# Kernel optimization log

Measured on AMD Instinct MI355X. Metric: run time of the kernel, lower is better.

## Reference

```python
import jax, jax.numpy as jnp
import numpy as np

NX = 2048
NL = 20
BATCH = 512
EIGMAX = 10.0
EPS = 1e-9


def prox_cardan(eta, x):
    """Prox of u -> -eta*(log(u)+log(1-u)) at x: unique root in (0,1) of
    u^3 - (1+x)u^2 + (x-2eta)u + eta = 0 (Cardano / trigonometric method)."""
    b = -(1.0 + x)
    c = x - 2.0 * eta
    d = eta
    p = c - b * b / 3.0
    q = 2.0 * b ** 3 / 27.0 - b * c / 3.0 + d
    disc = -4.0 * p ** 3 - 27.0 * q ** 2
    # three-real-roots branch (trigonometric); requires p<0
    pm = jnp.minimum(p, -1e-12)
    m = 2.0 * jnp.sqrt(-pm / 3.0)
    arg = jnp.clip(3.0 * q / (pm * m), -1.0, 1.0)
    th = jnp.arccos(arg)
    k = jnp.arange(3, dtype=x.dtype)
    t_trig = m[..., None] * jnp.cos((th[..., None] - 2.0 * jnp.pi * k) / 3.0)
    r_trig = t_trig - b[..., None] / 3.0
    in01 = (r_trig > 0.0) & (r_trig < 1.0)
    idx = jnp.argmax(in01, axis=-1)
    root3 = jnp.take_along_axis(r_trig, idx[..., None], axis=-1)[..., 0]
    # one-real-root branch
    s = jnp.sqrt(jnp.maximum(q * q / 4.0 + p ** 3 / 27.0, 0.0))
    root1 = jnp.cbrt(-q / 2.0 + s) + jnp.cbrt(-q / 2.0 - s) - b / 3.0
    u = jnp.where(disc >= 0.0, root3, root1)
    return jnp.clip(u, EPS, 1.0 - EPS)


def setup_inputs() -> dict:
    key = jax.random.key(0)
    k1, k2, k3, k4, k5 = jax.random.split(key, 5)
    x = jax.random.uniform(k1, (BATCH, 1, NX), dtype=jnp.float32)
    # symmetric PSD operators for T^T T and D^T D (as in a discretized inverse problem)
    A = jax.random.normal(k2, (NX, NX), dtype=jnp.float32)
    tTT = (A @ A.T) / NX
    B = jax.random.normal(k3, (NX, NX), dtype=jnp.float32)
    tDD = (B @ B.T) / NX
    # orthogonal change-of-basis: element <-> eigen bases
    Q, _ = jnp.linalg.qr(jax.random.normal(k4, (NX, NX), dtype=jnp.float32))
    Pelt = Q.astype(jnp.float32)
    Peig = Q.T.astype(jnp.float32)
    x_b = jnp.einsum('ij,bcj->bci', tTT, x) + 0.01 * jax.random.normal(k5, (BATCH, 1, NX), dtype=jnp.float32)
    gamma = jnp.full((NL,), 0.1, dtype=jnp.float32)   # nn.Parameter([0.1])
    mu = jnp.zeros((NL,), dtype=jnp.float32)          # nn.Parameter([0.0])
    reg = jnp.full((NL,), 0.001, dtype=jnp.float32)   # noisy=True -> trainable 0.001
    return {"x": x, "x_b": x_b, "tDD": tDD, "tTT": tTT, "Peig": Peig,
            "Pelt": Pelt, "gamma": gamma, "mu": mu, "reg": reg}


def reference(x, x_b, tDD, tTT, Peig, Pelt, gamma, mu, reg):
    def step(xc, params):
        g_raw, mu_raw, reg_raw = params
        g = jax.nn.softplus(g_raw)
        mu_l = jax.nn.softplus(mu_raw) / 1e6
        reg_l = jax.nn.softplus(reg_raw) / (EIGMAX ** 2)
        grad = (jnp.einsum('ij,bcj->bci', tTT, xc) - x_b
                + reg_l * jnp.einsum('ij,bcj->bci', tDD, xc))
        xt = xc - g * grad
        xt = jnp.einsum('ij,bcj->bci', Pelt, xt)
        xt = prox_cardan(g * mu_l, xt)
        xt = jnp.einsum('ij,bcj->bci', Peig, xt)
        return xt, None

    out, _ = jax.lax.scan(step, x, (gamma, mu, reg))
    return out
```

## Files before the change

kernel.cpp:

```cpp
#include <hip/hip_runtime.h>
#include <math.h>

#define MDIM 512
#define NDIM 2048
#define KDIM 2048
#define NLAYERS 20

static const size_t MN = (size_t)MDIM * NDIM;
static const size_t OPN = (size_t)KDIM * KDIM;

using bf16x8 = __attribute__((ext_vector_type(8))) short;
using f32x4  = __attribute__((ext_vector_type(4))) float;

__device__ __forceinline__ double softplusd(double v) {
    return (v > 20.0) ? v : log1p(exp(v));
}

__device__ __forceinline__ float prox_cardan_f(float eta, float x) {
    const float b  = -(1.0f + x);
    const float c  = x - 2.0f * eta;
    const float dd = eta;
    const float p  = c - b * b * (1.0f / 3.0f);
    const float q  = 2.0f * b * b * b * (1.0f / 27.0f) - b * c * (1.0f / 3.0f) + dd;
    const float disc = -4.0f * p * p * p - 27.0f * q * q;
    const float pm = fminf(p, -1e-12f);
    const float mm = 2.0f * sqrtf(-pm * (1.0f / 3.0f));
    float arg = 3.0f * q / (pm * mm);
    arg = fminf(fmaxf(arg, -1.0f), 1.0f);
    const float th = acosf(arg);
    const float TWO_PI = 6.28318530717958647692f;
    const float r0 = mm * cosf(th * (1.0f / 3.0f)) - b * (1.0f / 3.0f);
    const float r1 = mm * cosf((th - TWO_PI) * (1.0f / 3.0f)) - b * (1.0f / 3.0f);
    const float r2 = mm * cosf((th - 2.0f * TWO_PI) * (1.0f / 3.0f)) - b * (1.0f / 3.0f);
    const bool in0 = (r0 > 0.0f) && (r0 < 1.0f);
    const bool in1 = (r1 > 0.0f) && (r1 < 1.0f);
    const bool in2 = (r2 > 0.0f) && (r2 < 1.0f);
    const float root3 = in0 ? r0 : (in1 ? r1 : (in2 ? r2 : r0));
    const float s = sqrtf(fmaxf(q * q * 0.25f + p * p * p * (1.0f / 27.0f), 0.0f));
    const float root1 = cbrtf(-q * 0.5f + s) + cbrtf(-q * 0.5f - s) - b * (1.0f / 3.0f);
    const float u = (disc >= 0.0f) ? root3 : root1;
    return fminf(fmaxf(u, 1e-9f), 1.0f - 1e-9f);
}

__device__ __forceinline__ double prox_newton_d(double eta, double x) {
    double u = (double)prox_cardan_f((float)eta, (float)x);
#pragma unroll
    for (int i = 0; i < 4; ++i) {
        const double um1 = u - 1.0;
        const double umx = u - x;
        const double P  = u * um1 * umx - eta * (2.0 * u - 1.0);
        const double dP = um1 * umx + u * umx + u * um1 - 2.0 * eta;
        u = u - P / dP;
        u = fmin(fmax(u, 1e-12), 1.0 - 1e-12);
    }
    return fmin(fmax(u, 1e-9), 1.0 - 1e-9);
}

__device__ __forceinline__ unsigned short f2bf(float f) {
    unsigned u = __float_as_uint(f);
    unsigned r = (u + 0x7FFFu + ((u >> 16) & 1u)) >> 16;
    return (unsigned short)r;
}
__device__ __forceinline__ float bf2f(unsigned short h) {
    return __uint_as_float(((unsigned)h) << 16);
}
__device__ __forceinline__ void split3f(float f, unsigned short& b1,
                                        unsigned short& b2, unsigned short& b3) {
    b1 = f2bf(f);
    const float r1 = f - bf2f(b1);
    b2 = f2bf(r1);
    const float r2 = r1 - bf2f(b2);
    b3 = f2bf(r2);
}

__global__ __launch_bounds__(256) void split3_op(
    const float* __restrict__ s1, const float* __restrict__ s2,
    const float* __restrict__ greg, int layer,
    unsigned short* __restrict__ p1, unsigned short* __restrict__ p2,
    unsigned short* __restrict__ p3) {
    const size_t i = ((size_t)blockIdx.x * 256 + threadIdx.x) * 4;
    float reglf = 0.0f;
    if (s2) reglf = (float)(softplusd((double)greg[layer]) * 0.01);
    const float4 a = *(const float4*)(s1 + i);
    float4 b = make_float4(0.f, 0.f, 0.f, 0.f);
    if (s2) b = *(const float4*)(s2 + i);
    ushort4 o1, o2, o3;
    split3f(fmaf(reglf, b.x, a.x), o1.x, o2.x, o3.x);
    split3f(fmaf(reglf, b.y, a.y), o1.y, o2.y, o3.y);
    split3f(fmaf(reglf, b.z, a.z), o1.z, o2.z, o3.z);
    split3f(fmaf(reglf, b.w, a.w), o1.w, o2.w, o3.w);
    *(ushort4*)(p1 + i) = o1;
    *(ushort4*)(p2 + i) = o2;
    *(ushort4*)(p3 + i) = o3;
}

__global__ __launch_bounds__(256) void split3_w(
    const float* __restrict__ s1, const float* __restrict__ s2,
    const float* __restrict__ greg, int layer,
    unsigned short* __restrict__ p1, unsigned short* __restrict__ p2,
    unsigned short* __restrict__ p3) {
    if (layer > 0 && greg[layer] == greg[0]) return;
    const size_t i = ((size_t)blockIdx.x * 256 + threadIdx.x) * 4;
    const float reglf = (float)(softplusd((double)greg[layer]) * 0.01);
    const float4 a = *(const float4*)(s1 + i);
    const float4 b = *(const float4*)(s2 + i);
    ushort4 o1, o2, o3;
    split3f(fmaf(reglf, b.x, a.x), o1.x, o2.x, o3.x);
    split3f(fmaf(reglf, b.y, a.y), o1.y, o2.y, o3.y);
    split3f(fmaf(reglf, b.z, a.z), o1.z, o2.z, o3.z);
    split3f(fmaf(reglf, b.w, a.w), o1.w, o2.w, o3.w);
    *(ushort4*)(p1 + i) = o1;
    *(ushort4*)(p2 + i) = o2;
    *(ushort4*)(p3 + i) = o3;
}

__global__ __launch_bounds__(256, 2) void gemm_bf16x3(
    const unsigned short* __restrict__ A1, const unsigned short* __restrict__ A2,
    const unsigned short* __restrict__ A3,
    const unsigned short* __restrict__ W1, const unsigned short* __restrict__ W2,
    const unsigned short* __restrict__ W3,
    float* __restrict__ Part, int klen, int S) {
    __shared__ __align__(16) unsigned short Ab[3][64][64];
    __shared__ __align__(16) unsigned short Wb[3][64][64];

    const int tid = threadIdx.x;

    const int nwg = 256 * S;
    const int cpx = nwg >> 3;
    const int bid = blockIdx.x;
    const int g   = (bid & 7) * cpx + (bid >> 3);
    const int xs  = g / (8 * S);
    const int rr  = g - xs * (8 * S);
    const int ys  = rr & 7;
    const int zs  = rr >> 3;
    const int n0 = xs * 64;
    const int m0 = ys * 64;
    const int kb = zs * klen;

    const int lane = tid & 63, wid = tid >> 6;
    const int quad = lane >> 4, lrow = lane & 15;
    const int wm = (wid >> 1) * 32, wn = (wid & 1) * 32;

    const int srow = tid >> 2;
    const int sc   = tid & 3;
    const int sswz = srow & 7;
    const int rswz = lrow & 7;

    const unsigned short* gA1 = A1 + (size_t)(m0 + srow) * KDIM + kb + sc * 8;
    const unsigned short* gA2 = A2 + (size_t)(m0 + srow) * KDIM + kb + sc * 8;
    const unsigned short* gA3 = A3 + (size_t)(m0 + srow) * KDIM + kb + sc * 8;
    const unsigned short* gW1 = W1 + (size_t)(n0 + srow) * KDIM + kb + sc * 8;
    const unsigned short* gW2 = W2 + (size_t)(n0 + srow) * KDIM + kb + sc * 8;
    const unsigned short* gW3 = W3 + (size_t)(n0 + srow) * KDIM + kb + sc * 8;

    f32x4 ahi[2][2], alo[2][2];
#pragma unroll
    for (int a = 0; a < 2; ++a)
#pragma unroll
        for (int b2 = 0; b2 < 2; ++b2) {
            ahi[a][b2] = (f32x4){0.f, 0.f, 0.f, 0.f};
            alo[a][b2] = (f32x4){0.f, 0.f, 0.f, 0.f};
        }

    bf16x8 ra[3][2], rw[3][2];
#pragma unroll
    for (int h = 0; h < 2; ++h) {
        ra[0][h] = *(const bf16x8*)(gA1 + h * 32);
        ra[1][h] = *(const bf16x8*)(gA2 + h * 32);
        ra[2][h] = *(const bf16x8*)(gA3 + h * 32);
        rw[0][h] = *(const bf16x8*)(gW1 + h * 32);
        rw[1][h] = *(const bf16x8*)(gW2 + h * 32);
        rw[2][h] = *(const bf16x8*)(gW3 + h * 32);
    }

    const int nref = klen >> 6;

    for (int r = 0; r < nref; ++r) {
        __syncthreads();
#pragma unroll
        for (int h = 0; h < 2; ++h) {
            const int gp = (((sc + 4 * h) ^ sswz) * 8);
            *(bf16x8*)&Ab[0][srow][gp] = ra[0][h];
            *(bf16x8*)&Ab[1][srow][gp] = ra[1][h];
            *(bf16x8*)&Ab[2][srow][gp] = ra[2][h];
            *(bf16x8*)&Wb[0][srow][gp] = rw[0][h];
            *(bf16x8*)&Wb[1][srow][gp] = rw[1][h];
            *(bf16x8*)&Wb[2][srow][gp] = rw[2][h];
        }
        __syncthreads();

        if (r + 1 < nref) {
            const int ko = (r + 1) * 64;
#pragma unroll
            for (int h = 0; h < 2; ++h) {
                ra[0][h] = *(const bf16x8*)(gA1 + ko + h * 32);
                ra[1][h] = *(const bf16x8*)(gA2 + ko + h * 32);
                ra[2][h] = *(const bf16x8*)(gA3 + ko + h * 32);
                rw[0][h] = *(const bf16x8*)(gW1 + ko + h * 32);
                rw[1][h] = *(const bf16x8*)(gW2 + ko + h * 32);
                rw[2][h] = *(const bf16x8*)(gW3 + ko + h * 32);
            }
        }

#pragma unroll
        for (int kk = 0; kk < 2; ++kk) {
            bf16x8 fa[2][3], fw[2][3];
#pragma unroll
            for (int t = 0; t < 2; ++t) {
                const int raw = wm + t * 16 + lrow;
                const int rww = wn + t * 16 + lrow;
                const int gp = (((kk * 4 + quad) ^ rswz) * 8);
                fa[t][0] = *(const bf16x8*)&Ab[0][raw][gp];
                fa[t][1] = *(const bf16x8*)&Ab[1][raw][gp];
                fa[t][2] = *(const bf16x8*)&Ab[2][raw][gp];
                fw[t][0] = *(const bf16x8*)&Wb[0][rww][gp];
                fw[t][1] = *(const bf16x8*)&Wb[1][rww][gp];
                fw[t][2] = *(const bf16x8*)&Wb[2][rww][gp];
            }
            __builtin_amdgcn_s_setprio(1);
#pragma unroll
            for (int tm = 0; tm < 2; ++tm)
#pragma unroll
                for (int tn = 0; tn < 2; ++tn) {
                    ahi[tm][tn] = __builtin_amdgcn_mfma_f32_16x16x32_bf16(fa[tm][0], fw[tn][0], ahi[tm][tn], 0, 0, 0);
                    alo[tm][tn] = __builtin_amdgcn_mfma_f32_16x16x32_bf16(fa[tm][0], fw[tn][1], alo[tm][tn], 0, 0, 0);
                    alo[tm][tn] = __builtin_amdgcn_mfma_f32_16x16x32_bf16(fa[tm][1], fw[tn][0], alo[tm][tn], 0, 0, 0);
                    alo[tm][tn] = __builtin_amdgcn_mfma_f32_16x16x32_bf16(fa[tm][1], fw[tn][1], alo[tm][tn], 0, 0, 0);
                    alo[tm][tn] = __builtin_amdgcn_mfma_f32_16x16x32_bf16(fa[tm][0], fw[tn][2], alo[tm][tn], 0, 0, 0);
                    alo[tm][tn] = __builtin_amdgcn_mfma_f32_16x16x32_bf16(fa[tm][2], fw[tn][0], alo[tm][tn], 0, 0, 0);
                }
            __builtin_amdgcn_s_setprio(0);
        }
    }

    float* P = Part + (size_t)zs * MN;
#pragma unroll
    for (int tm = 0; tm < 2; ++tm)
#pragma unroll
        for (int tn = 0; tn < 2; ++tn) {
            const int mbase = m0 + wm + tm * 16 + quad * 4;
            const int nn = n0 + wn + tn * 16 + lrow;
#pragma unroll
            for (int r2 = 0; r2 < 4; ++r2)
                P[(size_t)(mbase + r2) * NDIM + nn] = ahi[tm][tn][r2] + alo[tm][tn][r2];
        }
}

template <int MODE>
__global__ __launch_bounds__(256) void combine3(
    const float* __restrict__ Part, int S,
    const float* __restrict__ Xc, const float* __restrict__ Xb,
    float* __restrict__ stateOut,
    unsigned short* __restrict__ p1, unsigned short* __restrict__ p2,
    unsigned short* __restrict__ p3,
    const float* __restrict__ gam, const float* __restrict__ gmu,
    const float* __restrict__ greg, int layer) {
    const size_t i = ((size_t)blockIdx.x * 256 + threadIdx.x) * 4;
    double s0 = 0.0, s1 = 0.0, s2 = 0.0, s3 = 0.0;
    for (int z = 0; z < S; ++z) {
        const float4 p = *(const float4*)(Part + (size_t)z * MN + i);
        s0 += (double)p.x; s1 += (double)p.y; s2 += (double)p.z; s3 += (double)p.w;
    }
    float v0, v1, v2, v3;
    if (MODE == 0) {
        const double g = softplusd((double)gam[layer]);
        const float4 xc = *(const float4*)(Xc + i);
        const float4 xb = *(const float4*)(Xb + i);
        v0 = (float)((double)xc.x - g * (s0 - (double)xb.x));
        v1 = (float)((double)xc.y - g * (s1 - (double)xb.y));
        v2 = (float)((double)xc.z - g * (s2 - (double)xb.z));
        v3 = (float)((double)xc.w - g * (s3 - (double)xb.w));
    } else if (MODE == 1) {
        const double g   = softplusd((double)gam[layer]);
        const double eta = g * softplusd((double)gmu[layer]) * 1e-6;
        v0 = (float)prox_newton_d(eta, s0);
        v1 = (float)prox_newton_d(eta, s1);
        v2 = (float)prox_newton_d(eta, s2);
        v3 = (float)prox_newton_d(eta, s3);
    } else {
        v0 = (float)s0; v1 = (float)s1; v2 = (float)s2; v3 = (float)s3;
        *(float4*)(stateOut + i) = make_float4(v0, v1, v2, v3);
    }
    ushort4 o1, o2, o3;
    split3f(v0, o1.x, o2.x, o3.x);
    split3f(v1, o1.y, o2.y, o3.y);
    split3f(v2, o1.z, o2.z, o3.z);
    split3f(v3, o1.w, o2.w, o3.w);
    *(ushort4*)(p1 + i) = o1;
    *(ushort4*)(p2 + i) = o2;
    *(ushort4*)(p3 + i) = o3;
}

#define BM 64
#define BN 64
#define BK 32
#define LDSP 68

__device__ __forceinline__ double prox_cardan_d(double eta, double x) {
    const double b  = -(1.0 + x);
    const double c  = x - 2.0 * eta;
    const double dd = eta;
    const double p  = c - b * b * (1.0 / 3.0);
    const double q  = 2.0 * b * b * b * (1.0 / 27.0) - b * c * (1.0 / 3.0) + dd;
    const double disc = -4.0 * p * p * p - 27.0 * q * q;
    const double pm = fmin(p, -1e-12);
    const double mm = 2.0 * sqrt(-pm * (1.0 / 3.0));
    double arg = 3.0 * q / (pm * mm);
    arg = fmin(fmax(arg, -1.0), 1.0);
    const double th = acos(arg);
    const double TWO_PI = 6.283185307179586476925286766559;
    const double r0 = mm * cos(th * (1.0 / 3.0)) - b * (1.0 / 3.0);
    const double r1 = mm * cos((th - TWO_PI) * (1.0 / 3.0)) - b * (1.0 / 3.0);
    const double r2 = mm * cos((th - 2.0 * TWO_PI) * (1.0 / 3.0)) - b * (1.0 / 3.0);
    const bool in0 = (r0 > 0.0) && (r0 < 1.0);
    const bool in1 = (r1 > 0.0) && (r1 < 1.0);
    const bool in2 = (r2 > 0.0) && (r2 < 1.0);
    const double root3 = in0 ? r0 : (in1 ? r1 : (in2 ? r2 : r0));
    const double s = sqrt(fmax(q * q * 0.25 + p * p * p * (1.0 / 27.0), 0.0));
    const double root1 = cbrt(-q * 0.5 + s) + cbrt(-q * 0.5 - s) - b * (1.0 / 3.0);
    const double u = (disc >= 0.0) ? root3 : root1;
    return fmin(fmax(u, 1e-9), 1.0 - 1e-9);
}

template <bool FUSE2>
__global__ __launch_bounds__(256, 4) void gemm_nt_splitk(
    const float* __restrict__ A, const float* __restrict__ W1,
    const float* __restrict__ W2, double* __restrict__ Part,
    const float* __restrict__ greg, int layer, int klen) {
    __shared__ float As[BK][LDSP];
    __shared__ float Ws[BK][LDSP];
    const int tid = threadIdx.x;
    const int m0 = blockIdx.y * BM;
    const int n0 = blockIdx.x * BN;
    const int kbase = blockIdx.z * klen;
    float reglf = 0.0f;
    if (FUSE2) reglf = (float)(softplusd((double)greg[layer]) * 0.01);
    const int lrow = tid >> 3;
    const int lkc  = (tid & 7) << 2;
    const float* pA  = A  + (size_t)(m0 + lrow) * KDIM + kbase + lkc;
    const float* pW  = W1 + (size_t)(n0 + lrow) * KDIM + kbase + lkc;
    const float* pW2 = FUSE2 ? (W2 + (size_t)(n0 + lrow) * KDIM + kbase + lkc) : nullptr;
    float4 ra[2], rw[2];
    ra[0] = *(const float4*)(pA);
    ra[1] = *(const float4*)(pA + 32 * KDIM);
    rw[0] = *(const float4*)(pW);
    rw[1] = *(const float4*)(pW + 32 * KDIM);
    if (FUSE2) {
        const float4 u0 = *(const float4*)(pW2);
        const float4 u1 = *(const float4*)(pW2 + 32 * KDIM);
        rw[0].x += reglf * u0.x; rw[0].y += reglf * u0.y;
        rw[0].z += reglf * u0.z; rw[0].w += reglf * u0.w;
        rw[1].x += reglf * u1.x; rw[1].y += reglf * u1.y;
        rw[1].z += reglf * u1.z; rw[1].w += reglf * u1.w;
    }
    float  acc[4][4]   = {};
    double acc64[4][4] = {};
    const int tx = (tid & 15) << 2;
    const int ty = (tid >> 4) << 2;
    int it = 0;
    for (int k0 = 0; k0 < klen; k0 += BK, ++it) {
#pragma unroll
        for (int h = 0; h < 2; ++h) {
            const int row = lrow + (h << 5);
            As[lkc + 0][row] = (h ? ra[1].x : ra[0].x);
            As[lkc + 1][row] = (h ? ra[1].y : ra[0].y);
            As[lkc + 2][row] = (h ? ra[1].z : ra[0].z);
            As[lkc + 3][row] = (h ? ra[1].w : ra[0].w);
            Ws[lkc + 0][row] = (h ? rw[1].x : rw[0].x);
            Ws[lkc + 1][row] = (h ? rw[1].y : rw[0].y);
            Ws[lkc + 2][row] = (h ? rw[1].z : rw[0].z);
            Ws[lkc + 3][row] = (h ? rw[1].w : rw[0].w);
        }
        __syncthreads();
        if (k0 + BK < klen) {
            const float* qA = pA + k0 + BK;
            ra[0] = *(const float4*)(qA);
            ra[1] = *(const float4*)(qA + 32 * KDIM);
            const float* qW = pW + k0 + BK;
            rw[0] = *(const float4*)(qW);
            rw[1] = *(const float4*)(qW + 32 * KDIM);
            if (FUSE2) {
                const float* qW2 = pW2 + k0 + BK;
                const float4 u0 = *(const float4*)(qW2);
                const float4 u1 = *(const float4*)(qW2 + 32 * KDIM);
                rw[0].x += reglf * u0.x; rw[0].y += reglf * u0.y;
                rw[0].z += reglf * u0.z; rw[0].w += reglf * u0.w;
                rw[1].x += reglf * u1.x; rw[1].y += reglf * u1.y;
                rw[1].z += reglf * u1.z; rw[1].w += reglf * u1.w;
            }
        }
#pragma unroll
        for (int kk = 0; kk < BK; ++kk) {
            const float4 a4 = *(const float4*)(&As[kk][ty]);
            const float4 b4 = *(const float4*)(&Ws[kk][tx]);
            const float av[4] = {a4.x, a4.y, a4.z, a4.w};
            const float bv[4] = {b4.x, b4.y, b4.z, b4.w};
#pragma unroll
            for (int r = 0; r < 4; ++r)
#pragma unroll
                for (int cc = 0; cc < 4; ++cc)
                    acc[r][cc] = fmaf(av[r], bv[cc], acc[r][cc]);
        }
        __syncthreads();
        if ((it & 1) == 1) {
#pragma unroll
            for (int r = 0; r < 4; ++r)
#pragma unroll
                for (int cc = 0; cc < 4; ++cc) {
                    acc64[r][cc] += (double)acc[r][cc];
                    acc[r][cc] = 0.0f;
                }
        }
    }
#pragma unroll
    for (int r = 0; r < 4; ++r)
#pragma unroll
        for (int cc = 0; cc < 4; ++cc)
            acc64[r][cc] += (double)acc[r][cc];
    double* Pz = Part + (size_t)blockIdx.z * MN;
#pragma unroll
    for (int r = 0; r < 4; ++r) {
        double* q = Pz + (size_t)(m0 + ty + r) * NDIM + n0 + tx;
        *(double2*)(q)     = make_double2(acc64[r][0], acc64[r][1]);
        *(double2*)(q + 2) = make_double2(acc64[r][2], acc64[r][3]);
    }
}

template <int MODE>
__global__ __launch_bounds__(256) void combine_ep(
    const double* __restrict__ Part, int nslices,
    const float* __restrict__ Xc, const float* __restrict__ Xb,
    float* __restrict__ Out,
    const float* __restrict__ gam, const float* __restrict__ gmu,
    const float* __restrict__ greg, int layer) {
    const size_t i4 = ((size_t)blockIdx.x * 256 + threadIdx.x) * 4;
    double s0 = 0.0, s1 = 0.0, s2 = 0.0, s3 = 0.0;
    for (int z = 0; z < nslices; ++z) {
        const double* p = Part + (size_t)z * MN + i4;
        const double2 a = *(const double2*)(p);
        const double2 b = *(const double2*)(p + 2);
        s0 += a.x; s1 += a.y; s2 += b.x; s3 += b.y;
    }
    float4 o;
    if (MODE == 0) {
        const double g = softplusd((double)gam[layer]);
        const float4 xc = *(const float4*)(Xc + i4);
        const float4 xb = *(const float4*)(Xb + i4);
        o.x = (float)((double)xc.x - g * (s0 - (double)xb.x));
        o.y = (float)((double)xc.y - g * (s1 - (double)xb.y));
        o.z = (float)((double)xc.z - g * (s2 - (double)xb.z));
        o.w = (float)((double)xc.w - g * (s3 - (double)xb.w));
    } else if (MODE == 1) {
        const double g   = softplusd((double)gam[layer]);
        const double eta = g * softplusd((double)gmu[layer]) * 1e-6;
        o.x = (float)prox_cardan_d(eta, s0);
        o.y = (float)prox_cardan_d(eta, s1);
        o.z = (float)prox_cardan_d(eta, s2);
        o.w = (float)prox_cardan_d(eta, s3);
    } else {
        o.x = (float)s0; o.y = (float)s1; o.z = (float)s2; o.w = (float)s3;
    }
    *(float4*)(Out + i4) = o;
}

extern "C" void kernel_launch(void* const* d_in, const int* in_sizes, int n_in,
                              void* d_out, int out_size, void* d_ws, size_t ws_size,
                              hipStream_t stream) {
    const float* x    = (const float*)d_in[0];
    const float* x_b  = (const float*)d_in[1];
    const float* tDD  = (const float*)d_in[2];
    const float* tTT  = (const float*)d_in[3];
    const float* Peig = (const float*)d_in[4];
    const float* Pelt = (const float*)d_in[5];
    const float* gam  = (const float*)d_in[6];
    const float* gmu  = (const float*)d_in[7];
    const float* greg = (const float*)d_in[8];
    float* out = (float*)d_out;

    const size_t TRI_OP_B = 3 * OPN * 2;
    const size_t TRI_A_B  = 3 * MN * 2;
    const size_t STATE_B  = MN * 4;
    const size_t full_need = 3 * TRI_OP_B + 2 * TRI_A_B + STATE_B + 2 * MN * 4;
    const size_t mid_need  = 1 * TRI_OP_B + 2 * TRI_A_B + STATE_B + 2 * MN * 4;

    const bool full = (ws_size >= full_need);
    const bool mid  = (!full && ws_size >= mid_need);

    if (full || mid) {
        const int S = 2;
        const int klen = KDIM / S;
        char* p = (char*)d_ws;
        unsigned short *Wt1, *Wt2, *Wt3, *Pe1, *Pe2, *Pe3, *Pg1, *Pg2, *Pg3;
        if (full) {
            Wt1 = (unsigned short*)p;        Wt2 = Wt1 + OPN; Wt3 = Wt2 + OPN; p += TRI_OP_B;
            Pe1 = (unsigned short*)p;        Pe2 = Pe1 + OPN; Pe3 = Pe2 + OPN; p += TRI_OP_B;
            Pg1 = (unsigned short*)p;        Pg2 = Pg1 + OPN; Pg3 = Pg2 + OPN; p += TRI_OP_B;
        } else {
            Wt1 = (unsigned short*)p;        Wt2 = Wt1 + OPN; Wt3 = Wt2 + OPN; p += TRI_OP_B;
            Pe1 = Wt1; Pe2 = Wt2; Pe3 = Wt3;
            Pg1 = Wt1; Pg2 = Wt2; Pg3 = Wt3;
        }
        unsigned short* Aa1 = (unsigned short*)p; unsigned short* Aa2 = Aa1 + MN;
        unsigned short* Aa3 = Aa2 + MN; p += TRI_A_B;
        unsigned short* Ab1 = (unsigned short*)p; unsigned short* Ab2 = Ab1 + MN;
        unsigned short* Ab3 = Ab2 + MN; p += TRI_A_B;
        float* state = (float*)p; p += STATE_B;
        float* part  = (float*)p;

        const dim3 gg((unsigned)(256 * S));
        const unsigned cgrid = (unsigned)(MN / 4 / 256);
        const unsigned ogrid = (unsigned)(OPN / 4 / 256);

        split3_op<<<cgrid, 256, 0, stream>>>(x, nullptr, greg, 0, Aa1, Aa2, Aa3);
        if (full) {
            split3_op<<<ogrid, 256, 0, stream>>>(Pelt, nullptr, greg, 0, Pe1, Pe2, Pe3);
            split3_op<<<ogrid, 256, 0, stream>>>(Peig, nullptr, greg, 0, Pg1, Pg2, Pg3);
        }

        unsigned short *c1 = Aa1, *c2 = Aa2, *c3 = Aa3;
        unsigned short *d1 = Ab1, *d2 = Ab2, *d3 = Ab3;

        for (int l = 0; l < NLAYERS; ++l) {
            if (full) {
                split3_w<<<ogrid, 256, 0, stream>>>(tTT, tDD, greg, l, Wt1, Wt2, Wt3);
            } else {
                split3_op<<<ogrid, 256, 0, stream>>>(tTT, tDD, greg, l, Wt1, Wt2, Wt3);
            }
            gemm_bf16x3<<<gg, 256, 0, stream>>>(c1, c2, c3, Wt1, Wt2, Wt3, part, klen, S);
            combine3<0><<<cgrid, 256, 0, stream>>>(part, S, (l == 0 ? x : state), x_b,
                                                   nullptr, d1, d2, d3, gam, gmu, greg, l);
            if (mid) split3_op<<<ogrid, 256, 0, stream>>>(Pelt, nullptr, greg, 0, Pe1, Pe2, Pe3);
            gemm_bf16x3<<<gg, 256, 0, stream>>>(d1, d2, d3, Pe1, Pe2, Pe3, part, klen, S);
            combine3<1><<<cgrid, 256, 0, stream>>>(part, S, nullptr, nullptr,
                                                   nullptr, c1, c2, c3, gam, gmu, greg, l);
            if (mid) split3_op<<<ogrid, 256, 0, stream>>>(Peig, nullptr, greg, 0, Pg1, Pg2, Pg3);
            gemm_bf16x3<<<gg, 256, 0, stream>>>(c1, c2, c3, Pg1, Pg2, Pg3, part, klen, S);
            combine3<2><<<cgrid, 256, 0, stream>>>(part, S, nullptr, nullptr,
                                                   (l == NLAYERS - 1 ? out : state),
                                                   d1, d2, d3, gam, gmu, greg, l);
            unsigned short* t;
            t = c1; c1 = d1; d1 = t;
            t = c2; c2 = d2; d2 = t;
            t = c3; c3 = d3; d3 = t;
        }
        return;
    }

    char* wsb = (char*)d_ws;
    float* b0 = (float*)wsb;
    float* b1 = b0 + MN;
    float* b2 = b1 + MN;
    float* b3 = b2 + MN;
    const size_t base_bytes = 4 * MN * sizeof(float);
    double* partd = (double*)(wsb + base_bytes);
    int S = 0;
    if (ws_size >= base_bytes + 2 * MN * sizeof(double)) S = 2;
    else if (ws_size >= base_bytes + 1 * MN * sizeof(double)) S = 1;
    if (S == 0) return;
    const int klen = KDIM / S;
    dim3 gg(NDIM / BN, MDIM / BM, S);
    dim3 cg((unsigned)(MN / 4 / 256));
    const float* cur = x;
    float* bx = b0; float* bu = b1; float* bn = b2; float* bo = b3;
    for (int l = 0; l < NLAYERS; ++l) {
        gemm_nt_splitk<true><<<gg, 256, 0, stream>>>(cur, tTT, tDD, partd, greg, l, klen);
        combine_ep<0><<<cg, 256, 0, stream>>>(partd, S, cur, x_b, bx, gam, gmu, greg, l);
        gemm_nt_splitk<false><<<gg, 256, 0, stream>>>(bx, Pelt, nullptr, partd, greg, l, klen);
        combine_ep<1><<<cg, 256, 0, stream>>>(partd, S, nullptr, nullptr, bu, gam, gmu, greg, l);
        gemm_nt_splitk<false><<<gg, 256, 0, stream>>>(bu, Peig, nullptr, partd, greg, l, klen);
        float* dst = (l == NLAYERS - 1) ? out : bn;
        combine_ep<2><<<cg, 256, 0, stream>>>(partd, S, nullptr, nullptr, dst, gam, gmu, greg, l);
        cur = bn;
        float* t = bn; bn = bo; bo = t;
    }
}
```

Measured before the change: 2.493 ms.

## Stage W tiles via direct global-to-LDS loads with double buffering

Replaces the register round-trip for the three W split operands with global_load_lds DMA into a double-buffered LDS tile, applying the XOR swizzle on the global source address. The next tile is fetched while MFMAs run on the current buffer, which cuts VGPR pressure and LDS store instructions. LDS use grows by half again, which may affect occupancy, and a full vmcnt wait still serializes the A register loads.

Result: no change. 2.476 ms (-0.7%).

```diff
diff --git a/kernel.cpp b/kernel.cpp
--- a/kernel.cpp
+++ b/kernel.cpp
@@ -73,6 +73,12 @@
     b3 = f2bf(r2);
 }
 
+__device__ __forceinline__ void gl16(const void* g, void* l) {
+    __builtin_amdgcn_global_load_lds(
+        (const __attribute__((address_space(1))) unsigned int*)g,
+        (__attribute__((address_space(3))) unsigned int*)l, 16, 0, 0);
+}
+
 __global__ __launch_bounds__(256) void split3_op(
     const float* __restrict__ s1, const float* __restrict__ s2,
     const float* __restrict__ greg, int layer,
@@ -121,7 +127,7 @@
     const unsigned short* __restrict__ W3,
     float* __restrict__ Part, int klen, int S) {
     __shared__ __align__(16) unsigned short Ab[3][64][64];
-    __shared__ __align__(16) unsigned short Wb[3][64][64];
+    __shared__ __align__(16) unsigned short Wb[2][3][64][64];
 
     const int tid = threadIdx.x;
 
@@ -149,9 +155,13 @@
     const unsigned short* gA1 = A1 + (size_t)(m0 + srow) * KDIM + kb + sc * 8;
     const unsigned short* gA2 = A2 + (size_t)(m0 + srow) * KDIM + kb + sc * 8;
     const unsigned short* gA3 = A3 + (size_t)(m0 + srow) * KDIM + kb + sc * 8;
-    const unsigned short* gW1 = W1 + (size_t)(n0 + srow) * KDIM + kb + sc * 8;
-    const unsigned short* gW2 = W2 + (size_t)(n0 + srow) * KDIM + kb + sc * 8;
-    const unsigned short* gW3 = W3 + (size_t)(n0 + srow) * KDIM + kb + sc * 8;
+
+    const int wrowt = tid >> 3;
+    const int wgc   = ((tid & 7) ^ (wrowt & 7)) * 8;
+    const unsigned short* gWp[3];
+    gWp[0] = W1 + (size_t)(n0 + wrowt) * KDIM + kb + wgc;
+    gWp[1] = W2 + (size_t)(n0 + wrowt) * KDIM + kb + wgc;
+    gWp[2] = W3 + (size_t)(n0 + wrowt) * KDIM + kb + wgc;
 
     f32x4 ahi[2][2], alo[2][2];
 #pragma unroll
@@ -162,19 +172,33 @@
             alo[a][b2] = (f32x4){0.f, 0.f, 0.f, 0.f};
         }
 
-    bf16x8 ra[3][2], rw[3][2];
-#pragma unroll
-    for (int h = 0; h < 2; ++h) {
-        ra[0][h] = *(const bf16x8*)(gA1 + h * 32);
-        ra[1][h] = *(const bf16x8*)(gA2 + h * 32);
-        ra[2][h] = *(const bf16x8*)(gA3 + h * 32);
-        rw[0][h] = *(const bf16x8*)(gW1 + h * 32);
-        rw[1][h] = *(const bf16x8*)(gW2 + h * 32);
-        rw[2][h] = *(const bf16x8*)(gW3 + h * 32);
-    }
+    bf16x8 ra[3][2];
+
+    auto loadA = [&](int r1) {
+        const int ko = r1 * 64;
+#pragma unroll
+        for (int h = 0; h < 2; ++h) {
+            ra[0][h] = *(const bf16x8*)(gA1 + ko + h * 32);
+            ra[1][h] = *(const bf16x8*)(gA2 + ko + h * 32);
+            ra[2][h] = *(const bf16x8*)(gA3 + ko + h * 32);
+        }
+    };
+    auto stageW = [&](int buf, int r1) {
+        const int ko = r1 * 64;
+#pragma unroll
+        for (int p = 0; p < 3; ++p)
+#pragma unroll
+            for (int h = 0; h < 2; ++h)
+                gl16(gWp[p] + (size_t)h * 32 * KDIM + ko,
+                     &Wb[buf][p][0][0] + ((size_t)h * 256 + tid) * 8);
+    };
 
     const int nref = klen >> 6;
 
+    loadA(0);
+    stageW(0, 0);
+
+    int buf = 0;
     for (int r = 0; r < nref; ++r) {
         __syncthreads();
 #pragma unroll
@@ -183,23 +207,13 @@
             *(bf16x8*)&Ab[0][srow][gp] = ra[0][h];
             *(bf16x8*)&Ab[1][srow][gp] = ra[1][h];
             *(bf16x8*)&Ab[2][srow][gp] = ra[2][h];
-            *(bf16x8*)&Wb[0][srow][gp] = rw[0][h];
-            *(bf16x8*)&Wb[1][srow][gp] = rw[1][h];
-            *(bf16x8*)&Wb[2][srow][gp] = rw[2][h];
-        }
+        }
+        asm volatile("s_waitcnt vmcnt(0)" ::: "memory");
         __syncthreads();
 
         if (r + 1 < nref) {
-            const int ko = (r + 1) * 64;
-#pragma unroll
-            for (int h = 0; h < 2; ++h) {
-                ra[0][h] = *(const bf16x8*)(gA1 + ko + h * 32);
-                ra[1][h] = *(const bf16x8*)(gA2 + ko + h * 32);
-                ra[2][h] = *(const bf16x8*)(gA3 + ko + h * 32);
-                rw[0][h] = *(const bf16x8*)(gW1 + ko + h * 32);
-                rw[1][h] = *(const bf16x8*)(gW2 + ko + h * 32);
-                rw[2][h] = *(const bf16x8*)(gW3 + ko + h * 32);
-            }
+            loadA(r + 1);
+            stageW(buf ^ 1, r + 1);
         }
 
 #pragma unroll
@@ -213,9 +227,9 @@
                 fa[t][0] = *(const bf16x8*)&Ab[0][raw][gp];
                 fa[t][1] = *(const bf16x8*)&Ab[1][raw][gp];
                 fa[t][2] = *(const bf16x8*)&Ab[2][raw][gp];
-                fw[t][0] = *(const bf16x8*)&Wb[0][rww][gp];
-                fw[t][1] = *(const bf16x8*)&Wb[1][rww][gp];
-                fw[t][2] = *(const bf16x8*)&Wb[2][rww][gp];
+                fw[t][0] = *(const bf16x8*)&Wb[buf][0][rww][gp];
+                fw[t][1] = *(const bf16x8*)&Wb[buf][1][rww][gp];
+                fw[t][2] = *(const bf16x8*)&Wb[buf][2][rww][gp];
             }
             __builtin_amdgcn_s_setprio(1);
 #pragma unroll
@@ -231,6 +245,7 @@
                 }
             __builtin_amdgcn_s_setprio(0);
         }
+        buf ^= 1;
     }
 
     float* P = Part + (size_t)zs * MN;
```
